# Optimization experiments

Hardware: AMD Instinct MI355X
Metric: run time of the kernel (lower is better)

The kernel has to match this reference:

```python
import jax, jax.numpy as jnp
import numpy as np


def setup_inputs() -> dict:
    key = jax.random.key(0)
    k1, k2 = jax.random.split(key)
    N, M, C = 8192, 16384, 128
    features = jax.random.normal(k1, (N, 1, 1, C), dtype=jnp.float32)
    patch_memory = jax.random.normal(k2, (1, M, 1, C), dtype=jnp.float32)
    return {"features": features, "patch_memory": patch_memory}


def reference(features, patch_memory):
    # Faithful to: torch.norm(features - patch_memory, dim=3); torch.min(dim=1)
    # features: [N, 1, 1, C], patch_memory: [1, M, 1, C] -> broadcast diff [N, M, 1, C]
    # Avoid materializing the [N, M, C] diff tensor: use the GEMM expansion
    # ||a-b||^2 = ||a||^2 + ||b||^2 - 2 a.b (same math, efficient form).
    f = features.reshape(features.shape[0], features.shape[-1])       # [N, C]
    m = patch_memory.reshape(patch_memory.shape[1], patch_memory.shape[-1])  # [M, C]
    f2 = jnp.sum(f * f, axis=-1)   # [N]
    m2 = jnp.sum(m * m, axis=-1)   # [M]
    cross = jnp.einsum('nc,mc->nm', f, m)  # [N, M]
    d2 = f2[:, None] + m2[None, :] - 2.0 * cross
    distances = jnp.sqrt(jnp.maximum(d2, 0.0))       # [N, M] == norm over dim 3
    min_distances = jnp.min(distances, axis=1)       # min over memory dim (dim=1)
    # original keeps the trailing singleton patch dim -> [N, 1]
    return min_distances[:, None]
```

## Files before the change

### kernel.cpp

```cpp
#include <hip/hip_runtime.h>
#include <hip/hip_bf16.h>
#include <stdint.h>

#define N_ROWS 8192
#define M_ROWS 16384
#define CDIM 128
#define NT 16

typedef unsigned short u16;
typedef __attribute__((ext_vector_type(2))) unsigned short u16x2;
typedef __attribute__((ext_vector_type(8))) short bf16x8;
typedef __attribute__((ext_vector_type(4))) float f32x4;

static __device__ __forceinline__ u16 f2bf(float x) {
  union { float f; uint32_t u; } v; v.f = x;
  uint32_t u = v.u;
  uint32_t r = u + 0x7FFFu + ((u >> 16) & 1u);
  return (u16)(r >> 16);
}
static __device__ __forceinline__ float bf2f(u16 b) {
  union { uint32_t u; float f; } v; v.u = ((uint32_t)b) << 16;
  return v.f;
}

__global__ __launch_bounds__(256) void prep_kernel(
    const float* __restrict__ f, const float* __restrict__ m,
    u16* __restrict__ fb, u16* __restrict__ mb,
    float* __restrict__ f2, float* __restrict__ m2, int* __restrict__ mind2)
{
  const int row = blockIdx.x * 4 + (threadIdx.x >> 6);
  const int lane = threadIdx.x & 63;
  const bool isF = row < N_ROWS;
  const float* src = isF ? (f + (size_t)row * CDIM)
                         : (m + (size_t)(row - N_ROWS) * CDIM);
  float2 v = *(const float2*)(src + lane * 2);
  u16 b0 = f2bf(v.x), b1 = f2bf(v.y);
  float x0 = bf2f(b0), x1 = bf2f(b1);
  float s = x0 * x0 + x1 * x1;
#pragma unroll
  for (int mask = 1; mask < 64; mask <<= 1)
    s += __shfl_xor(s, mask, 64);
  u16x2 bb = {b0, b1};
  if (isF) {
    *(u16x2*)(fb + (size_t)row * CDIM + lane * 2) = bb;
    if (lane == 0) { f2[row] = s; mind2[row] = 0x7F7FFFFF; }
  } else {
    const int r = row - N_ROWS;
    *(u16x2*)(mb + (size_t)r * CDIM + lane * 2) = bb;
    if (lane == 0) m2[r] = s;
  }
}

static __device__ __forceinline__ void stage_tile(const u16* __restrict__ src,
                                                  u16* __restrict__ dst, int tid) {
#pragma unroll
  for (int r = 0; r < 8; ++r) {
    const int t16 = r * 256 + tid;
    const int srcOff = (t16 ^ ((t16 >> 4) & 7)) * 8;
    const int dstOff = t16 * 8;
    __builtin_amdgcn_global_load_lds(
        (const __attribute__((address_space(1))) uint32_t*)(src + srcOff),
        (__attribute__((address_space(3))) uint32_t*)(dst + dstOff), 16, 0, 0);
  }
}

__global__ __launch_bounds__(256, 2) void gemm_min_kernel(
    const u16* __restrict__ fb, const u16* __restrict__ mb,
    const float* __restrict__ f2, const float* __restrict__ m2,
    int* __restrict__ mind2)
{
  __shared__ u16 smB[2][128 * 128];
  const int tid = threadIdx.x;
  const int msplit = blockIdx.x;
  const int nbase = blockIdx.y * 128;

  const int lane = tid & 63;
  const int w = tid >> 6;
  const int wr = w >> 1, wc = w & 1;
  const int l15 = lane & 15, l4 = lane >> 4;
  const int sw = (l15 & 7) << 4;

  stage_tile(fb + (size_t)nbase * CDIM, smB[1], tid);
  stage_tile(mb + (size_t)(msplit * NT) * 128 * CDIM, smB[0], tid);
  asm volatile("s_waitcnt vmcnt(0)" ::: "memory");
  __builtin_amdgcn_s_barrier();

  bf16x8 af[4][4];
#pragma unroll
  for (int mi = 0; mi < 4; ++mi)
#pragma unroll
    for (int ks = 0; ks < 4; ++ks) {
      const int row = wr * 64 + mi * 16 + l15;
      const int cb = (ks * 64 + l4 * 16) ^ sw;
      af[mi][ks] = *(const bf16x8*)&smB[1][row * 128 + (cb >> 1)];
    }
  __syncthreads();

  float tmin[4][4];
#pragma unroll
  for (int mi = 0; mi < 4; ++mi)
#pragma unroll
    for (int j = 0; j < 4; ++j) tmin[mi][j] = 3.0e38f;

  int cur = 0;
  for (int it = 0; it < NT; ++it) {
    const int mbase = (msplit * NT + it) * 128;
    if (it + 1 < NT) {
      stage_tile(mb + (size_t)(mbase + 128) * CDIM, smB[cur ^ 1], tid);
      asm volatile("s_waitcnt vmcnt(8)" ::: "memory");
    } else {
      asm volatile("s_waitcnt vmcnt(0)" ::: "memory");
    }
    __builtin_amdgcn_s_barrier();

    const u16* smcur = smB[cur];
    f32x4 acc[4][4];
#pragma unroll
    for (int mi = 0; mi < 4; ++mi)
#pragma unroll
      for (int ni = 0; ni < 4; ++ni) acc[mi][ni] = (f32x4){0.f, 0.f, 0.f, 0.f};

#pragma unroll
    for (int ks = 0; ks < 4; ++ks) {
      bf16x8 bg[4];
#pragma unroll
      for (int ni = 0; ni < 4; ++ni) {
        const int row = wc * 64 + ni * 16 + l15;
        const int cb = (ks * 64 + l4 * 16) ^ sw;
        bg[ni] = *(const bf16x8*)&smcur[row * 128 + (cb >> 1)];
      }
#pragma unroll
      for (int mi = 0; mi < 4; ++mi)
#pragma unroll
        for (int ni = 0; ni < 4; ++ni)
          acc[mi][ni] = __builtin_amdgcn_mfma_f32_16x16x32_bf16(
              af[mi][ks], bg[ni], acc[mi][ni], 0, 0, 0);
    }

#pragma unroll
    for (int ni = 0; ni < 4; ++ni) {
      const float m2v = m2[mbase + wc * 64 + ni * 16 + l15];
#pragma unroll
      for (int mi = 0; mi < 4; ++mi)
#pragma unroll
        for (int j = 0; j < 4; ++j)
          tmin[mi][j] = fminf(tmin[mi][j], fmaf(-2.0f, acc[mi][ni][j], m2v));
    }
    __syncthreads();
    cur ^= 1;
  }

#pragma unroll
  for (int mi = 0; mi < 4; ++mi)
#pragma unroll
    for (int j = 0; j < 4; ++j) {
      float t = tmin[mi][j];
      t = fminf(t, __shfl_xor(t, 1, 64));
      t = fminf(t, __shfl_xor(t, 2, 64));
      t = fminf(t, __shfl_xor(t, 4, 64));
      t = fminf(t, __shfl_xor(t, 8, 64));
      tmin[mi][j] = t;
    }
  if (l15 == 0) {
#pragma unroll
    for (int mi = 0; mi < 4; ++mi)
#pragma unroll
      for (int j = 0; j < 4; ++j) {
        const int row = nbase + wr * 64 + mi * 16 + l4 * 4 + j;
        const float d2 = fmaxf(f2[row] + tmin[mi][j], 0.0f);
        atomicMin(&mind2[row], __float_as_int(d2));
      }
  }
}

__global__ __launch_bounds__(256) void finalize_kernel(
    const int* __restrict__ mind2, float* __restrict__ out)
{
  const int i = blockIdx.x * 256 + threadIdx.x;
  out[i] = sqrtf(fmaxf(__int_as_float(mind2[i]), 0.0f));
}

extern "C" void kernel_launch(void* const* d_in, const int* in_sizes, int n_in,
                              void* d_out, int out_size, void* d_ws, size_t ws_size,
                              hipStream_t stream) {
  const float* f = (const float*)d_in[0];
  const float* m = (const float*)d_in[1];

  char* ws = (char*)d_ws;
  u16*  fb    = (u16*)(ws);
  u16*  mb    = (u16*)(ws + (2u << 20));
  float* f2   = (float*)(ws + (2u << 20) + (4u << 20));
  float* m2   = (float*)(ws + (2u << 20) + (4u << 20) + (32u << 10));
  int*  mind2 = (int*)(ws + (2u << 20) + (4u << 20) + (96u << 10));

  hipLaunchKernelGGL(prep_kernel, dim3((N_ROWS + M_ROWS) / 4), dim3(256), 0, stream,
                     f, m, fb, mb, f2, m2, mind2);
  hipLaunchKernelGGL(gemm_min_kernel, dim3(8, N_ROWS / 128), dim3(256), 0, stream,
                     fb, mb, f2, m2, mind2);
  hipLaunchKernelGGL(finalize_kernel, dim3(N_ROWS / 256), dim3(256), 0, stream,
                     mind2, (float*)d_out);
}
```

Measured before the change: 48.55 us.

## Interleave next-tile prefetch with MFMA k-steps and raise wave priority

The next memory tile's global-to-LDS loads are now split across the four k-steps of the MFMA loop, instead of being issued as one batch at the top of each iteration behind an explicit vmcnt wait and barrier. Each k-step adds an s_barrier and wraps its MFMA group in s_setprio to keep the waves in lockstep and favour matrix issue. The m2 values are loaded before the MFMAs, and the min update becomes a tree of fminf calls. The aim is to hide load latency and shorten the serial min chain, at the cost of more barriers per tile. Correctness now relies on the end-of-loop __syncthreads to drain outstanding loads before the next tile is read.

Result: no change. 49.06 us (+1.0%).

```diff
diff --git a/kernel.cpp b/kernel.cpp
--- a/kernel.cpp
+++ b/kernel.cpp
@@ -57,10 +57,9 @@
   for (int r = 0; r < 8; ++r) {
     const int t16 = r * 256 + tid;
     const int srcOff = (t16 ^ ((t16 >> 4) & 7)) * 8;
-    const int dstOff = t16 * 8;
     __builtin_amdgcn_global_load_lds(
         (const __attribute__((address_space(1))) uint32_t*)(src + srcOff),
-        (__attribute__((address_space(3))) uint32_t*)(dst + dstOff), 16, 0, 0);
+        (__attribute__((address_space(3))) uint32_t*)(dst + t16 * 8), 16, 0, 0);
   }
 }
 
@@ -105,15 +104,16 @@
   int cur = 0;
   for (int it = 0; it < NT; ++it) {
     const int mbase = (msplit * NT + it) * 128;
-    if (it + 1 < NT) {
-      stage_tile(mb + (size_t)(mbase + 128) * CDIM, smB[cur ^ 1], tid);
-      asm volatile("s_waitcnt vmcnt(8)" ::: "memory");
-    } else {
-      asm volatile("s_waitcnt vmcnt(0)" ::: "memory");
-    }
-    __builtin_amdgcn_s_barrier();
-
     const u16* smcur = smB[cur];
+    u16* smnxt = smB[cur ^ 1];
+    const u16* srcNext = mb + (size_t)(mbase + 128) * CDIM;
+    const bool pf = (it + 1 < NT);
+
+    float m2v[4];
+#pragma unroll
+    for (int ni = 0; ni < 4; ++ni)
+      m2v[ni] = m2[mbase + wc * 64 + ni * 16 + l15];
+
     f32x4 acc[4][4];
 #pragma unroll
     for (int mi = 0; mi < 4; ++mi)
@@ -122,6 +122,17 @@
 
 #pragma unroll
     for (int ks = 0; ks < 4; ++ks) {
+      if (pf) {
+#pragma unroll
+        for (int rr = 0; rr < 2; ++rr) {
+          const int t16 = (ks * 2 + rr) * 256 + tid;
+          const int srcOff = (t16 ^ ((t16 >> 4) & 7)) * 8;
+          __builtin_amdgcn_global_load_lds(
+              (const __attribute__((address_space(1))) uint32_t*)(srcNext + srcOff),
+              (__attribute__((address_space(3))) uint32_t*)(smnxt + t16 * 8),
+              16, 0, 0);
+        }
+      }
       bf16x8 bg[4];
 #pragma unroll
       for (int ni = 0; ni < 4; ++ni) {
@@ -129,23 +140,29 @@
         const int cb = (ks * 64 + l4 * 16) ^ sw;
         bg[ni] = *(const bf16x8*)&smcur[row * 128 + (cb >> 1)];
       }
+      __builtin_amdgcn_s_barrier();
+      __builtin_amdgcn_s_setprio(1);
 #pragma unroll
       for (int mi = 0; mi < 4; ++mi)
 #pragma unroll
         for (int ni = 0; ni < 4; ++ni)
           acc[mi][ni] = __builtin_amdgcn_mfma_f32_16x16x32_bf16(
               af[mi][ks], bg[ni], acc[mi][ni], 0, 0, 0);
+      __builtin_amdgcn_s_setprio(0);
     }
 
 #pragma unroll
-    for (int ni = 0; ni < 4; ++ni) {
-      const float m2v = m2[mbase + wc * 64 + ni * 16 + l15];
-#pragma unroll
-      for (int mi = 0; mi < 4; ++mi)
-#pragma unroll
-        for (int j = 0; j < 4; ++j)
-          tmin[mi][j] = fminf(tmin[mi][j], fmaf(-2.0f, acc[mi][ni][j], m2v));
-    }
+    for (int mi = 0; mi < 4; ++mi)
+#pragma unroll
+      for (int j = 0; j < 4; ++j) {
+        const float t0 = fmaf(-2.0f, acc[mi][0][j], m2v[0]);
+        const float t1 = fmaf(-2.0f, acc[mi][1][j], m2v[1]);
+        const float t2 = fmaf(-2.0f, acc[mi][2][j], m2v[2]);
+        const float t3 = fmaf(-2.0f, acc[mi][3][j], m2v[3]);
+        tmin[mi][j] = fminf(tmin[mi][j],
+                            fminf(fminf(t0, t1), fminf(t2, t3)));
+      }
+
     __syncthreads();
     cur ^= 1;
   }
```

## Fold -0.5*m2 into MFMA accumulator init and use 64-row double-buffered B tiles

Applied to the files above, without the earlier changes.

Prep now stores -0.5*||m||^2 per memory row. The GEMM kernel seeds the MFMA accumulators with that value, so each tile's epilogue reduces to a running max instead of an fma plus min, and -2 and f2 are applied once at the end. The M tile shrinks to 64 rows (twice as many iterations) with a single barrier per iteration. The per-block norm slice is preloaded into LDS, and s_setprio is raised around the MFMA block. The trade-off is more loop iterations, and the last iteration issues one redundant prefetch that wraps back to the first tile.

Measured after the change: 48.88 us. No clear change (+0.7%).

```diff
diff --git a/kernel.cpp b/kernel.cpp
--- a/kernel.cpp
+++ b/kernel.cpp
@@ -5,7 +5,8 @@
 #define N_ROWS 8192
 #define M_ROWS 16384
 #define CDIM 128
-#define NT 16
+#define NT 32
+#define BROWS 64
 
 typedef unsigned short u16;
 typedef __attribute__((ext_vector_type(2))) unsigned short u16x2;
@@ -26,7 +27,7 @@
 __global__ __launch_bounds__(256) void prep_kernel(
     const float* __restrict__ f, const float* __restrict__ m,
     u16* __restrict__ fb, u16* __restrict__ mb,
-    float* __restrict__ f2, float* __restrict__ m2, int* __restrict__ mind2)
+    float* __restrict__ f2, float* __restrict__ mh, int* __restrict__ mind2)
 {
   const int row = blockIdx.x * 4 + (threadIdx.x >> 6);
   const int lane = threadIdx.x & 63;
@@ -47,29 +48,17 @@
   } else {
     const int r = row - N_ROWS;
     *(u16x2*)(mb + (size_t)r * CDIM + lane * 2) = bb;
-    if (lane == 0) m2[r] = s;
-  }
-}
-
-static __device__ __forceinline__ void stage_tile(const u16* __restrict__ src,
-                                                  u16* __restrict__ dst, int tid) {
-#pragma unroll
-  for (int r = 0; r < 8; ++r) {
-    const int t16 = r * 256 + tid;
-    const int srcOff = (t16 ^ ((t16 >> 4) & 7)) * 8;
-    const int dstOff = t16 * 8;
-    __builtin_amdgcn_global_load_lds(
-        (const __attribute__((address_space(1))) uint32_t*)(src + srcOff),
-        (__attribute__((address_space(3))) uint32_t*)(dst + dstOff), 16, 0, 0);
+    if (lane == 0) mh[r] = -0.5f * s;
   }
 }
 
 __global__ __launch_bounds__(256, 2) void gemm_min_kernel(
     const u16* __restrict__ fb, const u16* __restrict__ mb,
-    const float* __restrict__ f2, const float* __restrict__ m2,
+    const float* __restrict__ f2, const float* __restrict__ mh,
     int* __restrict__ mind2)
 {
-  __shared__ u16 smB[2][128 * 128];
+  __shared__ __align__(16) u16 bts[2][BROWS * CDIM];
+  __shared__ __align__(16) float mhl[2048];
   const int tid = threadIdx.x;
   const int msplit = blockIdx.x;
   const int nbase = blockIdx.y * 128;
@@ -80,86 +69,127 @@
   const int l15 = lane & 15, l4 = lane >> 4;
   const int sw = (l15 & 7) << 4;
 
-  stage_tile(fb + (size_t)nbase * CDIM, smB[1], tid);
-  stage_tile(mb + (size_t)(msplit * NT) * 128 * CDIM, smB[0], tid);
+  int srcOffs[4], dstOffs[4];
+#pragma unroll
+  for (int c = 0; c < 4; ++c) {
+    const int t16 = c * 256 + tid;
+    srcOffs[c] = (t16 ^ ((t16 >> 4) & 7)) * 8;
+    dstOffs[c] = t16 * 8;
+  }
+
+  {
+    const u16* srcA = fb + (size_t)nbase * CDIM;
+    u16* base = &bts[0][0];
+#pragma unroll
+    for (int c = 0; c < 8; ++c) {
+      const int t16 = c * 256 + tid;
+      const int so = (t16 ^ ((t16 >> 4) & 7)) * 8;
+      __builtin_amdgcn_global_load_lds(
+          (const __attribute__((address_space(1))) uint32_t*)(srcA + so),
+          (__attribute__((address_space(3))) uint32_t*)(base + t16 * 8), 16, 0, 0);
+    }
+    const float* srcM = mh + msplit * 2048;
+#pragma unroll
+    for (int c = 0; c < 2; ++c) {
+      const int c16 = c * 256 + tid;
+      __builtin_amdgcn_global_load_lds(
+          (const __attribute__((address_space(1))) uint32_t*)(srcM + c16 * 4),
+          (__attribute__((address_space(3))) uint32_t*)(&mhl[c16 * 4]), 16, 0, 0);
+    }
+  }
   asm volatile("s_waitcnt vmcnt(0)" ::: "memory");
   __builtin_amdgcn_s_barrier();
 
   bf16x8 af[4][4];
+  {
+    const u16* base = &bts[0][0];
+#pragma unroll
+    for (int mi = 0; mi < 4; ++mi)
+#pragma unroll
+      for (int ks = 0; ks < 4; ++ks) {
+        const int row = wr * 64 + mi * 16 + l15;
+        const int cb = (ks * 64 + l4 * 16) ^ sw;
+        af[mi][ks] = *(const bf16x8*)&base[row * CDIM + (cb >> 1)];
+      }
+  }
+  __syncthreads();
+
+  {
+    const u16* srcB = mb + (size_t)(msplit * 2048) * CDIM;
+    u16* dstB = &bts[0][0];
+#pragma unroll
+    for (int c = 0; c < 4; ++c)
+      __builtin_amdgcn_global_load_lds(
+          (const __attribute__((address_space(1))) uint32_t*)(srcB + srcOffs[c]),
+          (__attribute__((address_space(3))) uint32_t*)(dstB + dstOffs[c]), 16, 0, 0);
+  }
+
+  float tmax[4][4];
 #pragma unroll
   for (int mi = 0; mi < 4; ++mi)
 #pragma unroll
+    for (int j = 0; j < 4; ++j) tmax[mi][j] = -3.0e38f;
+
+  for (int t = 0; t < NT; ++t) {
+    __builtin_amdgcn_s_barrier();
+    asm volatile("" ::: "memory");
+    {
+      const int tn = (t + 1) & (NT - 1);
+      const u16* srcB = mb + (size_t)(msplit * 2048 + tn * BROWS) * CDIM;
+      u16* dstB = &bts[(t + 1) & 1][0];
+#pragma unroll
+      for (int c = 0; c < 4; ++c)
+        __builtin_amdgcn_global_load_lds(
+            (const __attribute__((address_space(1))) uint32_t*)(srcB + srcOffs[c]),
+            (__attribute__((address_space(3))) uint32_t*)(dstB + dstOffs[c]), 16, 0, 0);
+    }
+    asm volatile("s_waitcnt vmcnt(4)" ::: "memory");
+
+    const u16* bt = &bts[t & 1][0];
+    const int brow0 = wc * 32 + l15;
+    const float mh0 = mhl[t * BROWS + brow0];
+    const float mh1 = mhl[t * BROWS + brow0 + 16];
+
+    f32x4 acc[4][2];
+#pragma unroll
+    for (int mi = 0; mi < 4; ++mi) {
+      acc[mi][0] = (f32x4){mh0, mh0, mh0, mh0};
+      acc[mi][1] = (f32x4){mh1, mh1, mh1, mh1};
+    }
+
+    __builtin_amdgcn_s_setprio(1);
+#pragma unroll
     for (int ks = 0; ks < 4; ++ks) {
-      const int row = wr * 64 + mi * 16 + l15;
       const int cb = (ks * 64 + l4 * 16) ^ sw;
-      af[mi][ks] = *(const bf16x8*)&smB[1][row * 128 + (cb >> 1)];
-    }
-  __syncthreads();
-
-  float tmin[4][4];
+      const bf16x8 bg0 = *(const bf16x8*)&bt[brow0 * CDIM + (cb >> 1)];
+      const bf16x8 bg1 = *(const bf16x8*)&bt[(brow0 + 16) * CDIM + (cb >> 1)];
+#pragma unroll
+      for (int mi = 0; mi < 4; ++mi) {
+        acc[mi][0] = __builtin_amdgcn_mfma_f32_16x16x32_bf16(
+            af[mi][ks], bg0, acc[mi][0], 0, 0, 0);
+        acc[mi][1] = __builtin_amdgcn_mfma_f32_16x16x32_bf16(
+            af[mi][ks], bg1, acc[mi][1], 0, 0, 0);
+      }
+    }
+    __builtin_amdgcn_s_setprio(0);
+
+#pragma unroll
+    for (int mi = 0; mi < 4; ++mi)
+#pragma unroll
+      for (int j = 0; j < 4; ++j)
+        tmax[mi][j] = fmaxf(tmax[mi][j], fmaxf(acc[mi][0][j], acc[mi][1][j]));
+  }
+
 #pragma unroll
   for (int mi = 0; mi < 4; ++mi)
 #pragma unroll
-    for (int j = 0; j < 4; ++j) tmin[mi][j] = 3.0e38f;
-
-  int cur = 0;
-  for (int it = 0; it < NT; ++it) {
-    const int mbase = (msplit * NT + it) * 128;
-    if (it + 1 < NT) {
-      stage_tile(mb + (size_t)(mbase + 128) * CDIM, smB[cur ^ 1], tid);
-      asm volatile("s_waitcnt vmcnt(8)" ::: "memory");
-    } else {
-      asm volatile("s_waitcnt vmcnt(0)" ::: "memory");
-    }
-    __builtin_amdgcn_s_barrier();
-
-    const u16* smcur = smB[cur];
-    f32x4 acc[4][4];
-#pragma unroll
-    for (int mi = 0; mi < 4; ++mi)
-#pragma unroll
-      for (int ni = 0; ni < 4; ++ni) acc[mi][ni] = (f32x4){0.f, 0.f, 0.f, 0.f};
-
-#pragma unroll
-    for (int ks = 0; ks < 4; ++ks) {
-      bf16x8 bg[4];
-#pragma unroll
-      for (int ni = 0; ni < 4; ++ni) {
-        const int row = wc * 64 + ni * 16 + l15;
-        const int cb = (ks * 64 + l4 * 16) ^ sw;
-        bg[ni] = *(const bf16x8*)&smcur[row * 128 + (cb >> 1)];
-      }
-#pragma unroll
-      for (int mi = 0; mi < 4; ++mi)
-#pragma unroll
-        for (int ni = 0; ni < 4; ++ni)
-          acc[mi][ni] = __builtin_amdgcn_mfma_f32_16x16x32_bf16(
-              af[mi][ks], bg[ni], acc[mi][ni], 0, 0, 0);
-    }
-
-#pragma unroll
-    for (int ni = 0; ni < 4; ++ni) {
-      const float m2v = m2[mbase + wc * 64 + ni * 16 + l15];
-#pragma unroll
-      for (int mi = 0; mi < 4; ++mi)
-#pragma unroll
-        for (int j = 0; j < 4; ++j)
-          tmin[mi][j] = fminf(tmin[mi][j], fmaf(-2.0f, acc[mi][ni][j], m2v));
-    }
-    __syncthreads();
-    cur ^= 1;
-  }
-
-#pragma unroll
-  for (int mi = 0; mi < 4; ++mi)
-#pragma unroll
     for (int j = 0; j < 4; ++j) {
-      float t = tmin[mi][j];
-      t = fminf(t, __shfl_xor(t, 1, 64));
-      t = fminf(t, __shfl_xor(t, 2, 64));
-      t = fminf(t, __shfl_xor(t, 4, 64));
-      t = fminf(t, __shfl_xor(t, 8, 64));
-      tmin[mi][j] = t;
+      float tv = tmax[mi][j];
+      tv = fmaxf(tv, __shfl_xor(tv, 1, 64));
+      tv = fmaxf(tv, __shfl_xor(tv, 2, 64));
+      tv = fmaxf(tv, __shfl_xor(tv, 4, 64));
+      tv = fmaxf(tv, __shfl_xor(tv, 8, 64));
+      tmax[mi][j] = tv;
     }
   if (l15 == 0) {
 #pragma unroll
@@ -167,7 +197,7 @@
 #pragma unroll
       for (int j = 0; j < 4; ++j) {
         const int row = nbase + wr * 64 + mi * 16 + l4 * 4 + j;
-        const float d2 = fmaxf(f2[row] + tmin[mi][j], 0.0f);
+        const float d2 = fmaxf(fmaf(-2.0f, tmax[mi][j], f2[row]), 0.0f);
         atomicMin(&mind2[row], __float_as_int(d2));
       }
   }
@@ -190,13 +220,13 @@
   u16*  fb    = (u16*)(ws);
   u16*  mb    = (u16*)(ws + (2u << 20));
   float* f2   = (float*)(ws + (2u << 20) + (4u << 20));
-  float* m2   = (float*)(ws + (2u << 20) + (4u << 20) + (32u << 10));
+  float* mh   = (float*)(ws + (2u << 20) + (4u << 20) + (32u << 10));
   int*  mind2 = (int*)(ws + (2u << 20) + (4u << 20) + (96u << 10));
 
   hipLaunchKernelGGL(prep_kernel, dim3((N_ROWS + M_ROWS) / 4), dim3(256), 0, stream,
-                     f, m, fb, mb, f2, m2, mind2);
+                     f, m, fb, mb, f2, mh, mind2);
   hipLaunchKernelGGL(gemm_min_kernel, dim3(8, N_ROWS / 128), dim3(256), 0, stream,
-                     fb, mb, f2, m2, mind2);
+                     fb, mb, f2, mh, mind2);
   hipLaunchKernelGGL(finalize_kernel, dim3(N_ROWS / 256), dim3(256), 0, stream,
                      mind2, (float*)d_out);
 }
```
